# Kernel tuning notes

Measured on AMD Instinct MI355X. Metric: run time of the kernel, lower is better.

The kernel has to match this reference:

```python
import jax, jax.numpy as jnp
import numpy as np

B, S, D, H = 2, 2048, 1024, 16
HD = D // H

def setup_inputs() -> dict:
    key = jax.random.key(0)
    ks = jax.random.split(key, 9)
    s = 1.0 / np.sqrt(D)
    inp = {"x": jax.random.normal(ks[0], (B, S, D), dtype=jnp.float32)}
    for i, name in enumerate(["q", "k", "v", "o"]):
        inp[f"W_{name}"] = jax.random.uniform(ks[1 + 2 * i], (D, D), dtype=jnp.float32, minval=-s, maxval=s)
        inp[f"b_{name}"] = jax.random.uniform(ks[2 + 2 * i], (D,), dtype=jnp.float32, minval=-s, maxval=s)
    return inp


def reference(x, W_q, b_q, W_k, b_k, W_v, b_v, W_o, b_o):
    # x: [B, S, D]
    def split_heads(t):
        return t.reshape(B, S, H, HD).transpose(0, 2, 1, 3)  # [B, H, S, HD]

    Q = split_heads(x @ W_q + b_q)
    K = split_heads(x @ W_k + b_k)
    V = split_heads(x @ W_v + b_v)

    scale = 1.0 / np.sqrt(HD).astype(np.float32)
    scores = jnp.einsum("bhqd,bhkd->bhqk", Q, K) * scale  # [B, H, S, S]
    weights = jax.nn.softmax(scores, axis=-1)
    attn = jnp.einsum("bhqk,bhkd->bhqd", weights, V)  # [B, H, S, HD]
    attn = attn.transpose(0, 2, 1, 3).reshape(B, S, D)
    return attn @ W_o + b_o
```

## Files before the change

kernel.cpp:

```cpp
#include <hip/hip_runtime.h>
#include <hip/hip_bf16.h>

#define BB 2
#define SS 2048
#define DD 1024
#define HH 16
#define HD 64

typedef __attribute__((ext_vector_type(8))) short bf16x8;
typedef __attribute__((ext_vector_type(4))) float f32x4;

__device__ __forceinline__ unsigned short f2bf(float f) {
  unsigned int u = __float_as_uint(f);
  return (unsigned short)((u + 0x7FFFu + ((u >> 16) & 1u)) >> 16);
}

__device__ __forceinline__ float fast_exp2(float x) {
#if __has_builtin(__builtin_amdgcn_exp2f)
  return __builtin_amdgcn_exp2f(x);
#else
  return __expf(x * 0.6931471805599453f);
#endif
}

__device__ __forceinline__ void async_copy16(const unsigned short* gp, unsigned short* lp) {
  __builtin_amdgcn_global_load_lds(
      (const __attribute__((address_space(1))) unsigned int*)gp,
      (__attribute__((address_space(3))) unsigned int*)lp, 16, 0, 0);
}

__device__ __forceinline__ void pl32_swap(unsigned& a, unsigned& b) {
#if __has_builtin(__builtin_amdgcn_permlane32_swap)
  auto r = __builtin_amdgcn_permlane32_swap(a, b, false, false);
  a = r[0];
  b = r[1];
#else
  asm volatile("v_permlane32_swap_b32 %0, %1" : "+v"(a), "+v"(b));
#endif
}
__device__ __forceinline__ void pl16_swap(unsigned& a, unsigned& b) {
#if __has_builtin(__builtin_amdgcn_permlane16_swap)
  auto r = __builtin_amdgcn_permlane16_swap(a, b, false, false);
  a = r[0];
  b = r[1];
#else
  asm volatile("v_permlane16_swap_b32 %0, %1" : "+v"(a), "+v"(b));
#endif
}

__global__ __launch_bounds__(256) void prep_kernel(
    const float* __restrict__ x, unsigned short* __restrict__ xb,
    const float* __restrict__ W0, unsigned short* __restrict__ T0,
    const float* __restrict__ W1, unsigned short* __restrict__ T1,
    const float* __restrict__ W2, unsigned short* __restrict__ T2,
    const float* __restrict__ W3, unsigned short* __restrict__ T3) {
  const int blk = blockIdx.x;
  const int t = threadIdx.x;
  if (blk < 4096) {
    int i = blk * 1024 + t * 4;
    float4 v = *(const float4*)(x + i);
    ushort4 u;
    u.x = f2bf(v.x); u.y = f2bf(v.y); u.z = f2bf(v.z); u.w = f2bf(v.w);
    *(ushort4*)(xb + i) = u;
    return;
  }
  const int j = blk - 4096;
  const int jw = j >> 10;
  const int tb = j & 1023;
  const float* W = jw == 0 ? W0 : (jw == 1 ? W1 : (jw == 2 ? W2 : W3));
  unsigned short* T = jw == 0 ? T0 : (jw == 1 ? T1 : (jw == 2 ? T2 : T3));
  __shared__ float tile[32][33];
  int k0 = (tb & 31) * 32, n0 = (tb >> 5) * 32;
  int c = t & 31, r0 = t >> 5;
#pragma unroll
  for (int i = 0; i < 4; ++i) {
    int r = r0 + i * 8;
    tile[r][c] = W[(size_t)(k0 + r) * DD + n0 + c];
  }
  __syncthreads();
#pragma unroll
  for (int i = 0; i < 4; ++i) {
    int r = r0 + i * 8;
    T[(size_t)(n0 + r) * DD + k0 + c] = f2bf(tile[c][r]);
  }
}

template <int STORE>
__device__ __forceinline__ void gemm_core(
    const unsigned short* __restrict__ A, const unsigned short* __restrict__ BT,
    const float* __restrict__ bias, void* __restrict__ outp, float scale,
    int bm, int bn) {
  const int t = threadIdx.x;
  const int w = t >> 6;
  const int l = t & 63;
  const int wm = (w >> 1) * 64;
  const int wn = (w & 1) * 64;

  __shared__ __align__(16) unsigned short As[128 * 32];
  __shared__ __align__(16) unsigned short Bs[128 * 32];

  f32x4 acc[4][4];
#pragma unroll
  for (int i = 0; i < 4; ++i)
#pragma unroll
    for (int j = 0; j < 4; ++j) acc[i][j] = (f32x4)0.f;

  const int fr = l & 15;
  const int kg = (l >> 4) * 8;

  for (int k0 = 0; k0 < DD; k0 += 32) {
    __syncthreads();
#pragma unroll
    for (int c = 0; c < 2; ++c) {
      int e = (w * 2 + c) * 512 + l * 8;
      int row = e >> 5, kk = e & 31;
      async_copy16(A + (size_t)(bm + row) * DD + k0 + kk, As + (w * 2 + c) * 512);
      async_copy16(BT + (size_t)(bn + row) * DD + k0 + kk, Bs + (w * 2 + c) * 512);
    }
    __syncthreads();

    bf16x8 af[4], bfr[4];
#pragma unroll
    for (int i = 0; i < 4; ++i)
      af[i] = *(const bf16x8*)(As + (wm + i * 16 + fr) * 32 + kg);
#pragma unroll
    for (int j = 0; j < 4; ++j)
      bfr[j] = *(const bf16x8*)(Bs + (wn + j * 16 + fr) * 32 + kg);
#pragma unroll
    for (int i = 0; i < 4; ++i)
#pragma unroll
      for (int j = 0; j < 4; ++j)
        acc[i][j] = __builtin_amdgcn_mfma_f32_16x16x32_bf16(af[i], bfr[j], acc[i][j], 0, 0, 0);
  }

  const int col_l = l & 15;
  const int row_l = (l >> 4) * 4;

  if (STORE == 2) {
    unsigned short* out = (unsigned short*)outp;
    unsigned int* T = (unsigned int*)As;
    const int b_ = bm >> 11;
    const int srow0 = bm & 2047;
#pragma unroll
    for (int p = 0; p < 4; ++p) {
      __syncthreads();
      if ((w & 1) == (p >> 1)) {
        const int jt0 = (p & 1) * 2;
#pragma unroll
        for (int jj = 0; jj < 2; ++jj) {
          int jt = jt0 + jj;
          int n_p = jj * 16 + col_l;
          float bv = bias[bn + p * 32 + n_p];
#pragma unroll
          for (int i = 0; i < 4; ++i) {
            int m0 = wm + i * 16 + row_l;
#pragma unroll
            for (int pr = 0; pr < 2; ++pr) {
              unsigned int val =
                  (unsigned int)f2bf(acc[i][jt][2 * pr] + bv) |
                  ((unsigned int)f2bf(acc[i][jt][2 * pr + 1] + bv) << 16);
              int m = m0 + 2 * pr;
              T[n_p * 64 + (((m >> 1)) ^ ((n_p & 7) << 2))] = val;
            }
          }
        }
      }
      __syncthreads();
#pragma unroll
      for (int c = 0; c < 2; ++c) {
        int q = t + c * 256;
        int n_p = q >> 4, cpos = q & 15;
        uint4 v = *(const uint4*)(T + n_p * 64 + ((cpos * 4) ^ ((n_p & 7) << 2)));
        int n_glob = bn + p * 32 + n_p;
        int h_ = n_glob >> 6, hd_ = n_glob & 63;
        *(uint4*)(out + ((size_t)((b_ * HH + h_) * HD + hd_)) * SS + srow0 + cpos * 8) = v;
      }
    }
    return;
  }

#pragma unroll
  for (int i = 0; i < 4; ++i) {
    int m_base = bm + wm + i * 16 + row_l;
#pragma unroll
    for (int j = 0; j < 4; ++j) {
      int n = bn + wn + j * 16 + col_l;
      float bv = bias[n];
      if (STORE == 0) {
        float* out = (float*)outp;
#pragma unroll
        for (int r = 0; r < 4; ++r)
          out[(size_t)(m_base + r) * DD + n] = acc[i][j][r] + bv;
      } else {
        unsigned short* out = (unsigned short*)outp;
        int h_ = n >> 6, hd_ = n & 63;
#pragma unroll
        for (int r = 0; r < 4; ++r) {
          int m = m_base + r;
          int b_ = m >> 11, s_ = m & 2047;
          out[(((size_t)(b_ * HH + h_) * SS) + s_) * HD + hd_] =
              f2bf((acc[i][j][r] + bv) * scale);
        }
      }
    }
  }
}

__global__ __launch_bounds__(256) void qkv_gemm_mfma(
    const unsigned short* __restrict__ A,
    const unsigned short* __restrict__ WqT, const unsigned short* __restrict__ WkT,
    const unsigned short* __restrict__ WvT,
    const float* __restrict__ bq, const float* __restrict__ bk,
    const float* __restrict__ bv,
    unsigned short* __restrict__ Qo, unsigned short* __restrict__ Ko,
    unsigned short* __restrict__ VTo) {
  const int i = blockIdx.x;
  const int xcd = i & 7;
  const int slot = i >> 3;
  const int bm = (xcd + 8 * (slot / 24)) * 128;
  const int c = slot % 24;
  const int which = c >> 3;
  const int bn = (c & 7) * 128;
  if (which == 0)
    gemm_core<1>(A, WqT, bq, (void*)Qo, 0.18033688011112042f, bm, bn);
  else if (which == 1)
    gemm_core<1>(A, WkT, bk, (void*)Ko, 1.0f, bm, bn);
  else
    gemm_core<2>(A, WvT, bv, (void*)VTo, 1.0f, bm, bn);
}

__global__ __launch_bounds__(256) void out_gemm_mfma(
    const unsigned short* __restrict__ A, const unsigned short* __restrict__ WoT,
    const float* __restrict__ bo, float* __restrict__ out) {
  const int i = blockIdx.x;
  const int xcd = i & 7;
  const int slot = i >> 3;
  const int bm = (xcd + 8 * (slot >> 3)) * 128;
  const int bn = (slot & 7) * 128;
  gemm_core<0>(A, WoT, bo, (void*)out, 1.0f, bm, bn);
}

__global__ __launch_bounds__(512, 4) void flash_attn_mfma(
    const unsigned short* __restrict__ Q,
    const unsigned short* __restrict__ K,
    const unsigned short* __restrict__ VT,
    unsigned short* __restrict__ ctx) {
  const int bh = blockIdx.x;
  const int qt = blockIdx.y;
  const int b  = bh >> 4;
  const int h  = bh & 15;
  const int t  = threadIdx.x;
  const int w  = t >> 6;
  const int l  = t & 63;
  const int wg = w & 3;
  const int wh = w >> 2;
  const int g  = l >> 4;
  const int ln = l & 15;

  const unsigned short* Qp = Q + ((size_t)bh * SS + (size_t)qt * 128 + wg * 32) * HD;
  const unsigned short* Kp = K + (size_t)bh * SS * HD;
  const unsigned short* Vp = VT + (size_t)bh * HD * SS;

  __shared__ __align__(16) unsigned short Ks[2][2][64 * 64];
  __shared__ __align__(16) unsigned short Vs[2][2][64 * 64];

  bf16x8 qf[2][2];
#pragma unroll
  for (int nt = 0; nt < 2; ++nt)
#pragma unroll
    for (int kb = 0; kb < 2; ++kb)
      qf[nt][kb] = *(const bf16x8*)(Qp + (nt * 16 + ln) * HD + kb * 32 + g * 8);

  f32x4 o[2][4];
#pragma unroll
  for (int nt = 0; nt < 2; ++nt)
#pragma unroll
    for (int mt = 0; mt < 4; ++mt) o[nt][mt] = (f32x4)0.f;
  float rs[2] = {0.f, 0.f};

  auto stage2 = [&](int kt2, int db) {
    const int c = t;
    const int row = c >> 3, cc = c & 7;
    const int gcc = cc ^ (row & 7);
    const int k0 = kt2 * 128;
    unsigned short* dK0 = &Ks[0][db][w * 512];
    unsigned short* dK1 = &Ks[1][db][w * 512];
    unsigned short* dV0 = &Vs[0][db][w * 512];
    unsigned short* dV1 = &Vs[1][db][w * 512];
    async_copy16(Kp + (size_t)(k0 + row) * HD + gcc * 8, dK0);
    async_copy16(Kp + (size_t)(k0 + 64 + row) * HD + gcc * 8, dK1);
    async_copy16(Vp + (size_t)row * SS + k0 + gcc * 8, dV0);
    async_copy16(Vp + (size_t)row * SS + k0 + 64 + gcc * 8, dV1);
  };

  stage2(0, 0);
  for (int kt2 = 0; kt2 < SS / 128; ++kt2) {
    const int db = kt2 & 1;
    __syncthreads();
    if (kt2 + 1 < SS / 128) stage2(kt2 + 1, db ^ 1);

    const unsigned short* Kst = &Ks[wh][db][0];
    const unsigned short* Vst = &Vs[wh][db][0];

    f32x4 st[2][4];
#pragma unroll
    for (int nt = 0; nt < 2; ++nt)
#pragma unroll
      for (int mt = 0; mt < 4; ++mt) st[nt][mt] = (f32x4)0.f;
#pragma unroll
    for (int kb = 0; kb < 2; ++kb)
#pragma unroll
      for (int mt = 0; mt < 4; ++mt) {
        int row = mt * 16 + ln;
        bf16x8 ka = *(const bf16x8*)(&Kst[row * 64 + (((kb * 4 + g) ^ (row & 7)) * 8)]);
        st[0][mt] = __builtin_amdgcn_mfma_f32_16x16x32_bf16(ka, qf[0][kb], st[0][mt], 0, 0, 0);
        st[1][mt] = __builtin_amdgcn_mfma_f32_16x16x32_bf16(ka, qf[1][kb], st[1][mt], 0, 0, 0);
      }

    unsigned Sd[2][4][2];
#pragma unroll
    for (int nt = 0; nt < 2; ++nt) {
#pragma unroll
      for (int mt = 0; mt < 4; ++mt) {
        float p0 = fast_exp2(st[nt][mt][0]);
        float p1 = fast_exp2(st[nt][mt][1]);
        float p2 = fast_exp2(st[nt][mt][2]);
        float p3 = fast_exp2(st[nt][mt][3]);
        Sd[nt][mt][0] = __builtin_amdgcn_perm(__float_as_uint(p1), __float_as_uint(p0),
                                              0x07060302u);
        Sd[nt][mt][1] = __builtin_amdgcn_perm(__float_as_uint(p3), __float_as_uint(p2),
                                              0x07060302u);
        rs[nt] += (p0 + p1) + (p2 + p3);
      }
#pragma unroll
      for (int m1 = 0; m1 < 2; ++m1)
#pragma unroll
        for (int p = 0; p < 2; ++p)
          pl32_swap(Sd[nt][2 * m1][p], Sd[nt][2 * m1 + 1][p]);
#pragma unroll
      for (int m1 = 0; m1 < 2; ++m1)
#pragma unroll
        for (int p = 0; p < 2; ++p)
          pl16_swap(Sd[nt][2 * m1][p], Sd[nt][2 * m1 + 1][p]);
    }

#pragma unroll
    for (int kb = 0; kb < 2; ++kb) {
      bf16x8 pbv[2];
#pragma unroll
      for (int nt = 0; nt < 2; ++nt) {
        union { unsigned u[4]; bf16x8 v; } c;
        c.u[0] = Sd[nt][2 * kb][0];
        c.u[1] = Sd[nt][2 * kb][1];
        c.u[2] = Sd[nt][2 * kb + 1][0];
        c.u[3] = Sd[nt][2 * kb + 1][1];
        pbv[nt] = c.v;
      }
#pragma unroll
      for (int mt = 0; mt < 4; ++mt) {
        int row = mt * 16 + ln;
        bf16x8 va = *(const bf16x8*)(&Vst[row * 64 + (((kb * 4 + g) ^ (row & 7)) * 8)]);
        o[0][mt] = __builtin_amdgcn_mfma_f32_16x16x32_bf16(va, pbv[0], o[0][mt], 0, 0, 0);
        o[1][mt] = __builtin_amdgcn_mfma_f32_16x16x32_bf16(va, pbv[1], o[1][mt], 0, 0, 0);
      }
    }
  }

  __syncthreads();
  {
    float* ored = (float*)&Vs[0][0][0];
    float* rred = (float*)&Ks[0][0][0];
    float* rb = ored + (wg * 64 + l) * 32;
    float* sb = rred + (wg * 64 + l) * 2;
    if (wh == 1) {
#pragma unroll
      for (int nt = 0; nt < 2; ++nt)
#pragma unroll
        for (int mt = 0; mt < 4; ++mt) {
          int idx = nt * 4 + mt;
          *(f32x4*)(rb + ((unsigned)(idx ^ (l & 7)) * 4)) = o[nt][mt];
        }
      sb[0] = rs[0];
      sb[1] = rs[1];
    }
    __syncthreads();
    if (wh == 1) return;
#pragma unroll
    for (int nt = 0; nt < 2; ++nt)
#pragma unroll
      for (int mt = 0; mt < 4; ++mt) {
        int idx = nt * 4 + mt;
        f32x4 pv = *(const f32x4*)(rb + ((unsigned)(idx ^ (l & 7)) * 4));
        o[nt][mt] += pv;
      }
    rs[0] += sb[0];
    rs[1] += sb[1];
  }

#pragma unroll
  for (int nt = 0; nt < 2; ++nt) {
    float lsum = rs[nt];
    lsum += __shfl_xor(lsum, 16, 64);
    lsum += __shfl_xor(lsum, 32, 64);
    float inv = 1.f / lsum;
    int srow = qt * 128 + wg * 32 + nt * 16 + ln;
    unsigned short* cb = ctx + (size_t)(b * SS + srow) * DD + h * HD;
#pragma unroll
    for (int mt = 0; mt < 4; ++mt) {
      ushort4 u4;
      u4.x = f2bf(o[nt][mt][0] * inv);
      u4.y = f2bf(o[nt][mt][1] * inv);
      u4.z = f2bf(o[nt][mt][2] * inv);
      u4.w = f2bf(o[nt][mt][3] * inv);
      *(ushort4*)(cb + mt * 16 + 4 * g) = u4;
    }
  }
}

extern "C" void kernel_launch(void* const* d_in, const int* in_sizes, int n_in,
                              void* d_out, int out_size, void* d_ws, size_t ws_size,
                              hipStream_t stream) {
  const float* x  = (const float*)d_in[0];
  const float* Wq = (const float*)d_in[1];
  const float* bq = (const float*)d_in[2];
  const float* Wk = (const float*)d_in[3];
  const float* bk = (const float*)d_in[4];
  const float* Wv = (const float*)d_in[5];
  const float* bv = (const float*)d_in[6];
  const float* Wo = (const float*)d_in[7];
  const float* bo = (const float*)d_in[8];
  float* out = (float*)d_out;

  const size_t ELEMS = (size_t)BB * SS * DD;
  char* ws = (char*)d_ws;
  unsigned short* xb   = (unsigned short*)ws;  ws += ELEMS * 2;
  unsigned short* WqT  = (unsigned short*)ws;  ws += (size_t)DD * DD * 2;
  unsigned short* WkT  = (unsigned short*)ws;  ws += (size_t)DD * DD * 2;
  unsigned short* WvT  = (unsigned short*)ws;  ws += (size_t)DD * DD * 2;
  unsigned short* WoT  = (unsigned short*)ws;  ws += (size_t)DD * DD * 2;
  unsigned short* Qb   = (unsigned short*)ws;  ws += ELEMS * 2;
  unsigned short* Kb   = (unsigned short*)ws;  ws += ELEMS * 2;
  unsigned short* VbT  = (unsigned short*)ws;  ws += ELEMS * 2;
  unsigned short* ctxb = (unsigned short*)ws;  ws += ELEMS * 2;

  prep_kernel<<<8192, 256, 0, stream>>>(x, xb, Wq, WqT, Wk, WkT, Wv, WvT, Wo, WoT);

  qkv_gemm_mfma<<<768, 256, 0, stream>>>(xb, WqT, WkT, WvT, bq, bk, bv,
                                         Qb, Kb, VbT);

  dim3 attn_grid(BB * HH, SS / 128);
  flash_attn_mfma<<<attn_grid, 512, 0, stream>>>(Qb, Kb, VbT, ctxb);

  out_gemm_mfma<<<256, 256, 0, stream>>>(ctxb, WoT, bo, out);
}
```

Before: 201.1 us.

## Rewrite QKV projection as 256x256-tile 8-phase pipelined MFMA GEMM

Replaces the 128x128-tile QKV GEMM (768 blocks of 256 threads) with a dedicated kernel that uses 256x256 tiles, 512 threads and 192 blocks. K-halves of A and B tiles are staged asynchronously into double-buffered, XOR-swizzled LDS. Each step is split into phases that interleave staging, explicit vmcnt waits, barriers and MFMA bursts run at raised priority. The aim is more data reuse per tile and better overlap of global loads with compute. The cost is fewer blocks than the 256 CUs, higher register pressure from 32 accumulators per thread, and delicate hand-written wait counts.

```diff
diff --git a/kernel.cpp b/kernel.cpp
--- a/kernel.cpp
+++ b/kernel.cpp
@@ -136,49 +136,6 @@
   const int col_l = l & 15;
   const int row_l = (l >> 4) * 4;
 
-  if (STORE == 2) {
-    unsigned short* out = (unsigned short*)outp;
-    unsigned int* T = (unsigned int*)As;
-    const int b_ = bm >> 11;
-    const int srow0 = bm & 2047;
-#pragma unroll
-    for (int p = 0; p < 4; ++p) {
-      __syncthreads();
-      if ((w & 1) == (p >> 1)) {
-        const int jt0 = (p & 1) * 2;
-#pragma unroll
-        for (int jj = 0; jj < 2; ++jj) {
-          int jt = jt0 + jj;
-          int n_p = jj * 16 + col_l;
-          float bv = bias[bn + p * 32 + n_p];
-#pragma unroll
-          for (int i = 0; i < 4; ++i) {
-            int m0 = wm + i * 16 + row_l;
-#pragma unroll
-            for (int pr = 0; pr < 2; ++pr) {
-              unsigned int val =
-                  (unsigned int)f2bf(acc[i][jt][2 * pr] + bv) |
-                  ((unsigned int)f2bf(acc[i][jt][2 * pr + 1] + bv) << 16);
-              int m = m0 + 2 * pr;
-              T[n_p * 64 + (((m >> 1)) ^ ((n_p & 7) << 2))] = val;
-            }
-          }
-        }
-      }
-      __syncthreads();
-#pragma unroll
-      for (int c = 0; c < 2; ++c) {
-        int q = t + c * 256;
-        int n_p = q >> 4, cpos = q & 15;
-        uint4 v = *(const uint4*)(T + n_p * 64 + ((cpos * 4) ^ ((n_p & 7) << 2)));
-        int n_glob = bn + p * 32 + n_p;
-        int h_ = n_glob >> 6, hd_ = n_glob & 63;
-        *(uint4*)(out + ((size_t)((b_ * HH + h_) * HD + hd_)) * SS + srow0 + cpos * 8) = v;
-      }
-    }
-    return;
-  }
-
 #pragma unroll
   for (int i = 0; i < 4; ++i) {
     int m_base = bm + wm + i * 16 + row_l;
@@ -186,27 +143,57 @@
     for (int j = 0; j < 4; ++j) {
       int n = bn + wn + j * 16 + col_l;
       float bv = bias[n];
-      if (STORE == 0) {
-        float* out = (float*)outp;
-#pragma unroll
-        for (int r = 0; r < 4; ++r)
-          out[(size_t)(m_base + r) * DD + n] = acc[i][j][r] + bv;
-      } else {
-        unsigned short* out = (unsigned short*)outp;
-        int h_ = n >> 6, hd_ = n & 63;
-#pragma unroll
-        for (int r = 0; r < 4; ++r) {
-          int m = m_base + r;
-          int b_ = m >> 11, s_ = m & 2047;
-          out[(((size_t)(b_ * HH + h_) * SS) + s_) * HD + hd_] =
-              f2bf((acc[i][j][r] + bv) * scale);
-        }
-      }
-    }
-  }
-}
-
-__global__ __launch_bounds__(256) void qkv_gemm_mfma(
+      float* out = (float*)outp;
+#pragma unroll
+      for (int r = 0; r < 4; ++r)
+        out[(size_t)(m_base + r) * DD + n] = acc[i][j][r] + bv;
+    }
+  }
+}
+
+__global__ __launch_bounds__(256) void out_gemm_mfma(
+    const unsigned short* __restrict__ A, const unsigned short* __restrict__ WoT,
+    const float* __restrict__ bo, float* __restrict__ out) {
+  const int i = blockIdx.x;
+  const int xcd = i & 7;
+  const int slot = i >> 3;
+  const int bm = (xcd + 8 * (slot >> 3)) * 128;
+  const int bn = (slot & 7) * 128;
+  gemm_core<0>(A, WoT, bo, (void*)out, 1.0f, bm, bn);
+}
+
+#define QPHASE(DB, KH, MH, S, VM) do {                                        \
+    bf16x8 af[4];                                                             \
+    _Pragma("unroll")                                                         \
+    for (int ii = 0; ii < 4; ++ii) {                                          \
+      int row = wm * 128 + (MH) * 64 + ii * 16 + fr;                          \
+      int kb = kg16 ^ ((row & 8) ? 32 : 0) ^ ((row & 4) ? 16 : 0);            \
+      af[ii] = *(const bf16x8*)((const char*)&lds[0][DB][KH][0] + row * 64 + kb); \
+    }                                                                         \
+    if ((MH) == 0) {                                                          \
+      _Pragma("unroll")                                                       \
+      for (int j = 0; j < 4; ++j) {                                           \
+        int row = wn * 64 + j * 16 + fr;                                      \
+        int kb = kg16 ^ ((row & 8) ? 32 : 0) ^ ((row & 4) ? 16 : 0);          \
+        bfr[j] = *(const bf16x8*)((const char*)&lds[1][DB][KH][0] + row * 64 + kb); \
+      }                                                                       \
+    }                                                                         \
+    stage_half(S);                                                            \
+    asm volatile("s_barrier" ::: "memory");                                   \
+    __builtin_amdgcn_s_setprio(1);                                            \
+    _Pragma("unroll")                                                         \
+    for (int ii = 0; ii < 4; ++ii)                                            \
+      _Pragma("unroll")                                                       \
+      for (int j = 0; j < 4; ++j)                                             \
+        acc[(MH) * 4 + ii][j] = __builtin_amdgcn_mfma_f32_16x16x32_bf16(      \
+            af[ii], bfr[j], acc[(MH) * 4 + ii][j], 0, 0, 0);                  \
+    __builtin_amdgcn_s_setprio(0);                                            \
+    if ((VM) == 1) asm volatile("s_waitcnt vmcnt(4)" ::: "memory");           \
+    if ((VM) == 2) asm volatile("s_waitcnt vmcnt(0)" ::: "memory");           \
+    asm volatile("s_barrier" ::: "memory");                                   \
+  } while (0)
+
+__global__ __launch_bounds__(512, 2) void qkv_gemm_8ph(
     const unsigned short* __restrict__ A,
     const unsigned short* __restrict__ WqT, const unsigned short* __restrict__ WkT,
     const unsigned short* __restrict__ WvT,
@@ -217,27 +204,130 @@
   const int i = blockIdx.x;
   const int xcd = i & 7;
   const int slot = i >> 3;
-  const int bm = (xcd + 8 * (slot / 24)) * 128;
-  const int c = slot % 24;
-  const int which = c >> 3;
-  const int bn = (c & 7) * 128;
-  if (which == 0)
-    gemm_core<1>(A, WqT, bq, (void*)Qo, 0.18033688011112042f, bm, bn);
-  else if (which == 1)
-    gemm_core<1>(A, WkT, bk, (void*)Ko, 1.0f, bm, bn);
-  else
-    gemm_core<2>(A, WvT, bv, (void*)VTo, 1.0f, bm, bn);
-}
-
-__global__ __launch_bounds__(256) void out_gemm_mfma(
-    const unsigned short* __restrict__ A, const unsigned short* __restrict__ WoT,
-    const float* __restrict__ bo, float* __restrict__ out) {
-  const int i = blockIdx.x;
-  const int xcd = i & 7;
-  const int slot = i >> 3;
-  const int bm = (xcd + 8 * (slot >> 3)) * 128;
-  const int bn = (slot & 7) * 128;
-  gemm_core<0>(A, WoT, bo, (void*)out, 1.0f, bm, bn);
+  const int bmi = xcd * 2 + (slot / 12);
+  const int c = slot % 12;
+  const int which = c >> 2;
+  const int bm = bmi * 256;
+  const int bn = (c & 3) * 256;
+  const unsigned short* BT = which == 0 ? WqT : (which == 1 ? WkT : WvT);
+  const float* bias = which == 0 ? bq : (which == 1 ? bk : bv);
+
+  const int t = threadIdx.x;
+  const int w = t >> 6;
+  const int l = t & 63;
+  const int wm = w >> 2;
+  const int wn = w & 3;
+  const int fr = l & 15;
+  const int kg16 = (l >> 4) * 16;
+
+  __shared__ __align__(16) unsigned short lds[2][2][2][8192];
+
+  f32x4 acc[8][4];
+#pragma unroll
+  for (int mi = 0; mi < 8; ++mi)
+#pragma unroll
+    for (int j = 0; j < 4; ++j) acc[mi][j] = (f32x4)0.f;
+
+  auto stage_half = [&](int s) {
+    if (s >= 64) return;
+    const int Ts = s >> 2;
+    const int db = Ts & 1;
+    const int typ = s & 3;
+    const int kh = typ >> 1;
+    const int isB = typ & 1;
+    const unsigned short* src = isB ? BT : A;
+    const int rbase = isB ? bn : bm;
+    unsigned short* dstbase = &lds[isB][db][kh][0];
+    const int k0 = Ts * 64 + kh * 32;
+#pragma unroll
+    for (int j = 0; j < 2; ++j) {
+      int cc = (w * 2 + j) * 64 + l;
+      int row = cc >> 2;
+      int ke = ((cc & 3) * 8) ^ ((row & 8) ? 16 : 0) ^ ((row & 4) ? 8 : 0);
+      async_copy16(src + (size_t)(rbase + row) * DD + k0 + ke,
+                   dstbase + (w * 2 + j) * 512);
+    }
+  };
+
+  bf16x8 bfr[4];
+
+  for (int s = 0; s < 6; ++s) stage_half(s);
+  asm volatile("s_waitcnt vmcnt(4)" ::: "memory");
+  asm volatile("s_barrier" ::: "memory");
+
+  for (int T = 0; T < 14; ++T) {
+    const int db = T & 1;
+    const int sb = 4 * T + 6;
+    QPHASE(db, 0, 0, sb + 0, 0);
+    QPHASE(db, 0, 1, sb + 1, 0);
+    QPHASE(db, 1, 0, sb + 2, 0);
+    QPHASE(db, 1, 1, sb + 3, 1);
+  }
+  QPHASE(0, 0, 0, 62, 0);
+  QPHASE(0, 0, 1, 63, 0);
+  QPHASE(0, 1, 0, 64, 0);
+  QPHASE(0, 1, 1, 64, 2);
+  QPHASE(1, 0, 0, 64, 0);
+  QPHASE(1, 0, 1, 64, 0);
+  QPHASE(1, 1, 0, 64, 0);
+  QPHASE(1, 1, 1, 64, 0);
+
+  const int col_l = l & 15;
+  const int row_l = (l >> 4) * 4;
+  const int b_ = bm >> 11;
+
+  if (which != 2) {
+    const float scl = which == 0 ? 0.18033688011112042f : 1.0f;
+    unsigned short* out = which == 0 ? Qo : Ko;
+#pragma unroll
+    for (int mi = 0; mi < 8; ++mi) {
+      int m_base = bm + wm * 128 + mi * 16 + row_l;
+#pragma unroll
+      for (int j = 0; j < 4; ++j) {
+        int n = bn + wn * 64 + j * 16 + col_l;
+        float bv = bias[n];
+        int h_ = n >> 6, hd_ = n & 63;
+#pragma unroll
+        for (int r = 0; r < 4; ++r) {
+          int m = m_base + r;
+          int b2 = m >> 11, s_ = m & 2047;
+          out[(((size_t)(b2 * HH + h_) * SS) + s_) * HD + hd_] =
+              f2bf((acc[mi][j][r] + bv) * scl);
+        }
+      }
+    }
+  } else {
+    unsigned int* Tt = (unsigned int*)&lds[0][0][0][0];
+#pragma unroll
+    for (int mi = 0; mi < 8; ++mi) {
+      int m2a = wm * 64 + mi * 8 + (l >> 4) * 2;
+#pragma unroll
+      for (int j = 0; j < 4; ++j) {
+        int n = wn * 64 + j * 16 + col_l;
+        float bv = bias[bn + n];
+        uint2 dd;
+        dd.x = (unsigned)f2bf(acc[mi][j][0] + bv) |
+               ((unsigned)f2bf(acc[mi][j][1] + bv) << 16);
+        dd.y = (unsigned)f2bf(acc[mi][j][2] + bv) |
+               ((unsigned)f2bf(acc[mi][j][3] + bv) << 16);
+        *(uint2*)(Tt + n * 128 + (m2a ^ ((n & 7) << 2))) = dd;
+      }
+    }
+    __syncthreads();
+    const int srow0 = bm & 2047;
+    const int n_r = t >> 1;
+    const int half = t & 1;
+    const int n_glob = bn + n_r;
+    const int h_ = n_glob >> 6, hd_ = n_glob & 63;
+    unsigned short* ob =
+        VTo + ((size_t)((b_ * HH + h_) * HD + hd_)) * SS + srow0 + half * 128;
+#pragma unroll
+    for (int cp = 0; cp < 16; ++cp) {
+      uint4 v = *(const uint4*)(Tt + n_r * 128 +
+                                ((half * 64 + cp * 4) ^ ((n_r & 7) << 2)));
+      *(uint4*)(ob + cp * 8) = v;
+    }
+  }
 }
 
 __global__ __launch_bounds__(512, 4) void flash_attn_mfma(
@@ -279,18 +369,14 @@
   float rs[2] = {0.f, 0.f};
 
   auto stage2 = [&](int kt2, int db) {
-    const int c = t;
-    const int row = c >> 3, cc = c & 7;
+    const int cidx = t;
+    const int row = cidx >> 3, cc = cidx & 7;
     const int gcc = cc ^ (row & 7);
     const int k0 = kt2 * 128;
-    unsigned short* dK0 = &Ks[0][db][w * 512];
-    unsigned short* dK1 = &Ks[1][db][w * 512];
-    unsigned short* dV0 = &Vs[0][db][w * 512];
-    unsigned short* dV1 = &Vs[1][db][w * 512];
-    async_copy16(Kp + (size_t)(k0 + row) * HD + gcc * 8, dK0);
-    async_copy16(Kp + (size_t)(k0 + 64 + row) * HD + gcc * 8, dK1);
-    async_copy16(Vp + (size_t)row * SS + k0 + gcc * 8, dV0);
-    async_copy16(Vp + (size_t)row * SS + k0 + 64 + gcc * 8, dV1);
+    async_copy16(Kp + (size_t)(k0 + row) * HD + gcc * 8, &Ks[0][db][w * 512]);
+    async_copy16(Kp + (size_t)(k0 + 64 + row) * HD + gcc * 8, &Ks[1][db][w * 512]);
+    async_copy16(Vp + (size_t)row * SS + k0 + gcc * 8, &Vs[0][db][w * 512]);
+    async_copy16(Vp + (size_t)row * SS + k0 + 64 + gcc * 8, &Vs[1][db][w * 512]);
   };
 
   stage2(0, 0);
@@ -349,12 +435,12 @@
       bf16x8 pbv[2];
 #pragma unroll
       for (int nt = 0; nt < 2; ++nt) {
-        union { unsigned u[4]; bf16x8 v; } c;
-        c.u[0] = Sd[nt][2 * kb][0];
-        c.u[1] = Sd[nt][2 * kb][1];
-        c.u[2] = Sd[nt][2 * kb + 1][0];
-        c.u[3] = Sd[nt][2 * kb + 1][1];
-        pbv[nt] = c.v;
+        union { unsigned u[4]; bf16x8 v; } cu;
+        cu.u[0] = Sd[nt][2 * kb][0];
+        cu.u[1] = Sd[nt][2 * kb][1];
+        cu.u[2] = Sd[nt][2 * kb + 1][0];
+        cu.u[3] = Sd[nt][2 * kb + 1][1];
+        pbv[nt] = cu.v;
       }
 #pragma unroll
       for (int mt = 0; mt < 4; ++mt) {
@@ -445,8 +531,8 @@
 
   prep_kernel<<<8192, 256, 0, stream>>>(x, xb, Wq, WqT, Wk, WkT, Wv, WvT, Wo, WoT);
 
-  qkv_gemm_mfma<<<768, 256, 0, stream>>>(xb, WqT, WkT, WvT, bq, bk, bv,
-                                         Qb, Kb, VbT);
+  qkv_gemm_8ph<<<192, 512, 0, stream>>>(xb, WqT, WkT, WvT, bq, bk, bv,
+                                        Qb, Kb, VbT);
 
   dim3 attn_grid(BB * HH, SS / 128);
   flash_attn_mfma<<<attn_grid, 512, 0, stream>>>(Qb, Kb, VbT, ctxb);
```

Result: faster. 194.2 us (-3.5%).
